# Kernel tuning notes

Measured on AMD Instinct MI355X. Metric: run time of the kernel, lower is better.

Reference implementation:

```python
import jax, jax.numpy as jnp
import numpy as np

B, CHAR_LEN, LSTM, VOCAB, NATTN = 4096, 64, 400, 73, 10

def _lstm_cell(x, h, c, W_ih, W_hh, b):
    # gates: [B, 4*LSTM] in (i, f, g, o) order, matching torch.nn.LSTMCell
    g = x @ W_ih.T + h @ W_hh.T + b
    i, f, gg, o = jnp.split(g, 4, axis=1)
    i = jax.nn.sigmoid(i); f = jax.nn.sigmoid(f)
    gg = jnp.tanh(gg); o = jax.nn.sigmoid(o)
    c_new = f * c + i * gg
    h_new = o * jnp.tanh(c_new)
    return h_new, c_new

def setup_inputs() -> dict:
    key = jax.random.key(0)
    ks = jax.random.split(key, 24)
    d = {}
    d['inputs'] = jax.random.normal(ks[0], (B, 3), jnp.float32)
    for n, k in zip(['h1','c1','h2','c2','h3','c3'], ks[1:7]):
        d[n] = jax.random.normal(k, (B, LSTM), jnp.float32) * 0.1
    d['kappa'] = jax.random.uniform(ks[7], (B, NATTN), jnp.float32) * 5.0
    d['w_prev'] = jax.random.uniform(ks[8], (B, VOCAB), jnp.float32)
    d['attention_values'] = jax.random.uniform(ks[9], (B, CHAR_LEN, VOCAB), jnp.float32)
    d['attention_lengths'] = jax.random.randint(ks[10], (B,), 1, CHAR_LEN + 1, jnp.int32)
    s = 0.05
    in1 = VOCAB + 3              # lstm1 input: [w, inputs]
    in23 = 3 + LSTM + VOCAB      # lstm2/3 input: [inputs, h, w]
    attn_in = VOCAB + 3 + LSTM
    d['W_ih1'] = jax.random.normal(ks[11], (4 * LSTM, in1), jnp.float32) * s
    d['W_hh1'] = jax.random.normal(ks[12], (4 * LSTM, LSTM), jnp.float32) * s
    d['b1'] = jax.random.normal(ks[13], (4 * LSTM,), jnp.float32) * s
    d['W_attn'] = jax.random.normal(ks[14], (3 * NATTN, attn_in), jnp.float32) * s
    d['b_attn'] = jax.random.normal(ks[15], (3 * NATTN,), jnp.float32) * s
    d['W_ih2'] = jax.random.normal(ks[16], (4 * LSTM, in23), jnp.float32) * s
    d['W_hh2'] = jax.random.normal(ks[17], (4 * LSTM, LSTM), jnp.float32) * s
    d['b2'] = jax.random.normal(ks[18], (4 * LSTM,), jnp.float32) * s
    d['W_ih3'] = jax.random.normal(ks[19], (4 * LSTM, in23), jnp.float32) * s
    d['W_hh3'] = jax.random.normal(ks[20], (4 * LSTM, LSTM), jnp.float32) * s
    d['b3'] = jax.random.normal(ks[21], (4 * LSTM,), jnp.float32) * s
    return d

def reference(inputs, h1, c1, h2, c2, h3, c3, kappa, w_prev, attention_values,
              attention_lengths, W_ih1, W_hh1, b1, W_attn, b_attn,
              W_ih2, W_hh2, b2, W_ih3, W_hh3, b3):
    char_len = attention_values.shape[1]
    # --- LSTM 1 ---
    s1_in = jnp.concatenate([w_prev, inputs], axis=1)
    h1n, c1n = _lstm_cell(s1_in, h1, c1, W_ih1, W_hh1, b1)
    # --- Gaussian-mixture location attention ---
    attn_in = jnp.concatenate([w_prev, inputs, h1n], axis=1)
    attn_params = jax.nn.softplus(attn_in @ W_attn.T + b_attn)
    alpha, beta, kap = jnp.split(attn_params, 3, axis=1)
    kap = kappa + kap / 25.0
    beta = jnp.maximum(beta, 0.01)
    u = jnp.arange(char_len, dtype=jnp.float32)[None, None, :]           # [1,1,C]
    phi = jnp.sum(alpha[:, :, None] *
                  jnp.exp(-jnp.square(kap[:, :, None] - u) / beta[:, :, None]),
                  axis=1)                                                 # [B,C]
    seq_mask = (jnp.arange(char_len)[None, :] < attention_lengths[:, None]).astype(jnp.float32)
    w = jnp.einsum('bc,bcv->bv', phi * seq_mask, attention_values)        # [B,V]
    # --- LSTM 2 & 3 ---
    s2_in = jnp.concatenate([inputs, h1n, w], axis=1)
    h2n, c2n = _lstm_cell(s2_in, h2, c2, W_ih2, W_hh2, b2)
    s3_in = jnp.concatenate([inputs, h2n, w], axis=1)
    h3n, c3n = _lstm_cell(s3_in, h3, c3, W_ih3, W_hh3, b3)
    return h3n
```

## Files before the change

kernel.cpp:

```cpp
#include <hip/hip_runtime.h>
#include <hip/hip_bf16.h>


#define B_SZ     4096
#define LSTM_N   400
#define NG       1600
#define NGP      1664
#define VOCAB    73
#define NATTN    10
#define CHARLEN  64
#define KP1      480
#define KP23     896

typedef _Float16 half8 __attribute__((ext_vector_type(8)));
typedef __attribute__((ext_vector_type(4))) float floatx4;

__device__ __forceinline__ void gload_lds16(const void* g, void* l) {
    __builtin_amdgcn_global_load_lds(
        (const __attribute__((address_space(1))) void*)g,
        (__attribute__((address_space(3))) void*)l, 16, 0, 0);
}

__device__ __forceinline__ int lds_slot(int r, int s) {
    return ((r >> 1) << 6) + (((((r & 1) << 2) | s) ^ ((r >> 1) & 7)) << 3);
}

__global__ __launch_bounds__(256) void pack_wall(const float* __restrict__ Wih1,
                                                 const float* __restrict__ Whh1,
                                                 const float* __restrict__ Wih2,
                                                 const float* __restrict__ Whh2,
                                                 const float* __restrict__ Wih3,
                                                 const float* __restrict__ Whh3,
                                                 const float* __restrict__ W_attn,
                                                 _Float16* __restrict__ W1,
                                                 _Float16* __restrict__ W2,
                                                 _Float16* __restrict__ W3,
                                                 _Float16* __restrict__ Wa)
{
    const int z = blockIdx.z;
    const int n = blockIdx.y;
    const int k = blockIdx.x * 256 + threadIdx.x;
    if (z == 0) {
        if (k >= KP1) return;
        float v = 0.f;
        if (n < NG) {
            if (k < 76)             v = Wih1[(size_t)n * 76 + k];
            else if (k < 476)       v = Whh1[(size_t)n * 400 + (k - 76)];
        }
        W1[(size_t)n * KP1 + k] = (_Float16)v;
    } else if (z == 1 || z == 2) {
        if (k >= KP23) return;
        const float* Wih = (z == 1) ? Wih2 : Wih3;
        const float* Whh = (z == 1) ? Whh2 : Whh3;
        float v = 0.f;
        if (n < NG) {
            if (k < 476)            v = Wih[(size_t)n * 476 + k];
            else if (k < 876)       v = Whh[(size_t)n * 400 + (k - 476)];
        }
        ((z == 1) ? W2 : W3)[(size_t)n * KP23 + k] = (_Float16)v;
    } else {
        if (n >= 128 || k >= KP1) return;
        float v = (n < 30 && k < 476) ? W_attn[(size_t)n * 476 + k] : 0.f;
        Wa[(size_t)n * KP1 + k] = (_Float16)v;
    }
}

__global__ __launch_bounds__(256) void pack_x(const float* __restrict__ w_prev,
                                              const float* __restrict__ inputs,
                                              const float* __restrict__ h1,
                                              const float* __restrict__ h2,
                                              const float* __restrict__ h3,
                                              _Float16* __restrict__ X1,
                                              _Float16* __restrict__ X2,
                                              _Float16* __restrict__ X3)
{
    const int b = blockIdx.y;
    const int k = blockIdx.x * 256 + threadIdx.x;
    if (k < KP1) {
        float v = 0.f;
        if (k < 73)        v = w_prev[(size_t)b * 73 + k];
        else if (k < 76)   v = inputs[(size_t)b * 3 + (k - 73)];
        else if (k < 476)  v = h1[(size_t)b * 400 + (k - 76)];
        X1[(size_t)b * KP1 + k] = (_Float16)v;
    }
    const int kk = k - KP1;
    if (kk >= 0 && kk < KP23) {
        if (kk >= 3 && kk < 476) return;
        float v2 = 0.f, v3 = 0.f;
        if (kk < 3) { v2 = inputs[(size_t)b * 3 + kk]; v3 = v2; }
        else if (kk >= 476 && kk < 876) {
            v2 = h2[(size_t)b * 400 + (kk - 476)];
            v3 = h3[(size_t)b * 400 + (kk - 476)];
        }
        X2[(size_t)b * KP23 + kk] = (_Float16)v2;
        X3[(size_t)b * KP23 + kk] = (_Float16)v3;
    }
}

__global__ __launch_bounds__(256) void gemm_f16(const _Float16* __restrict__ A,
                                                const _Float16* __restrict__ Bw,
                                                const float* __restrict__ bias,
                                                float* __restrict__ C, int Kp,
                                                int ldC, int Nvalid)
{
    __shared__ _Float16 As[128 * 32];
    __shared__ _Float16 Bs[128 * 32];

    const int t    = threadIdx.x;
    const int w    = t >> 6;
    const int lane = t & 63;
    const int quad = lane >> 4;
    const int l16  = lane & 15;
    const int m0   = blockIdx.y * 128;
    const int n0   = blockIdx.x * 128;
    const int wm   = (w >> 1) * 64;
    const int wn   = (w & 1) * 64;
    const int pr   = lane >> 3;
    const int sw8  = (lane & 7) ^ pr;
    const int rowo = (pr << 1) + (sw8 >> 2);
    const int ko   = (sw8 & 3) << 3;

    floatx4 acc[4][4] = {};

    for (int k0 = 0; k0 < Kp; k0 += 32) {
        __syncthreads();
#pragma unroll
        for (int j = 0; j < 2; j++) {
            const int cr = (j * 4 + w) * 16;
            gload_lds16(A  + (size_t)(m0 + cr + rowo) * Kp + k0 + ko, As + cr * 32);
            gload_lds16(Bw + (size_t)(n0 + cr + rowo) * Kp + k0 + ko, Bs + cr * 32);
        }
        asm volatile("s_waitcnt vmcnt(0)" ::: "memory");
        __syncthreads();

        half8 af[4], bf[4];
#pragma unroll
        for (int i = 0; i < 4; i++) {
            af[i] = *(const half8*)(As + lds_slot(wm + i * 16 + l16, quad));
            bf[i] = *(const half8*)(Bs + lds_slot(wn + i * 16 + l16, quad));
        }
#pragma unroll
        for (int mt = 0; mt < 4; mt++)
#pragma unroll
            for (int nt = 0; nt < 4; nt++)
                acc[mt][nt] = __builtin_amdgcn_mfma_f32_16x16x32_f16(
                    af[mt], bf[nt], acc[mt][nt], 0, 0, 0);
    }

#pragma unroll
    for (int nt = 0; nt < 4; nt++) {
        const int n = n0 + wn + nt * 16 + l16;
        if (n >= Nvalid) continue;
        const float bv = bias[n];
#pragma unroll
        for (int mt = 0; mt < 4; mt++) {
            const int mbase = m0 + wm + mt * 16 + quad * 4;
#pragma unroll
            for (int r = 0; r < 4; r++)
                C[(size_t)(mbase + r) * ldC + n] = acc[mt][nt][r] + bv;
        }
    }
}

__global__ __launch_bounds__(256) void gates_mid(const float* __restrict__ G,
                                                 const float* __restrict__ c_in,
                                                 _Float16* __restrict__ d1, int ld1,
                                                 _Float16* __restrict__ d2, int ld2)
{
    int id = blockIdx.x * 256 + threadIdx.x;
    if (id >= B_SZ * LSTM_N) return;
    int b = id / LSTM_N;
    int u = id - b * LSTM_N;
    const float* g = G + (size_t)b * NG;
    float gi = g[u], gf = g[LSTM_N + u], gc = g[2 * LSTM_N + u], go = g[3 * LSTM_N + u];
    float si = 1.f / (1.f + expf(-gi));
    float sf = 1.f / (1.f + expf(-gf));
    float so = 1.f / (1.f + expf(-go));
    float cn = sf * c_in[id] + si * tanhf(gc);
    float h  = so * tanhf(cn);
    _Float16 hh = (_Float16)h;
    d1[(size_t)b * ld1 + u] = hh;
    if (d2) d2[(size_t)b * ld2 + u] = hh;
}

__global__ __launch_bounds__(256) void gates_last(const float* __restrict__ G,
                                                  const float* __restrict__ c_in,
                                                  float* __restrict__ out)
{
    int id = blockIdx.x * 256 + threadIdx.x;
    if (id >= B_SZ * LSTM_N) return;
    int b = id / LSTM_N;
    int u = id - b * LSTM_N;
    const float* g = G + (size_t)b * NG;
    float gi = g[u], gf = g[LSTM_N + u], gc = g[2 * LSTM_N + u], go = g[3 * LSTM_N + u];
    float si = 1.f / (1.f + expf(-gi));
    float sf = 1.f / (1.f + expf(-gf));
    float so = 1.f / (1.f + expf(-go));
    float cn = sf * c_in[id] + si * tanhf(gc);
    out[id]  = so * tanhf(cn);
}

__global__ __launch_bounds__(256) void attn_phi(const float* __restrict__ AP,
                                                const float* __restrict__ kappa,
                                                const float* __restrict__ AV,
                                                const int* __restrict__ alen,
                                                _Float16* __restrict__ X2,
                                                _Float16* __restrict__ X3)
{
    __shared__ float prm[4][32];
    __shared__ float phi_s[4][CHARLEN];

    const int t = threadIdx.x;
    const int wave = t >> 6;
    const int lane = t & 63;
    const int b = blockIdx.x * 4 + wave;

    if (lane < 30) {
        float p  = AP[(size_t)b * 32 + lane];
        float sp = (p > 20.f) ? p : log1pf(expf(p));
        float v;
        if (lane < 10)      v = sp;
        else if (lane < 20) v = fmaxf(sp, 0.01f);
        else                v = kappa[(size_t)b * NATTN + (lane - 20)] + sp * (1.f / 25.f);
        prm[wave][lane] = v;
    }
    __syncthreads();

    const int len = alen[b];
    {
        int c = lane;
        float phi = 0.f;
#pragma unroll
        for (int j = 0; j < NATTN; j++) {
            float d = prm[wave][20 + j] - (float)c;
            phi += prm[wave][j] * expf(-d * d / prm[wave][10 + j]);
        }
        phi_s[wave][c] = (c < len) ? phi : 0.f;
    }
    __syncthreads();

    for (int v0 = 0; v0 < VOCAB; v0 += 64) {
        const int v = v0 + lane;
        if (v < VOCAB) {
            const float* avb = AV + (size_t)b * CHARLEN * VOCAB + v;
            float s = 0.f;
            for (int c = 0; c < len; c++)
                s += phi_s[wave][c] * avb[(size_t)c * VOCAB];
            _Float16 wv = (_Float16)s;
            X2[(size_t)b * KP23 + 403 + v] = wv;
            X3[(size_t)b * KP23 + 403 + v] = wv;
        }
    }
}

extern "C" void kernel_launch(void* const* d_in, const int* in_sizes, int n_in,
                              void* d_out, int out_size, void* d_ws, size_t ws_size,
                              hipStream_t stream)
{
    const float* inputs = (const float*)d_in[0];
    const float* h1     = (const float*)d_in[1];
    const float* c1     = (const float*)d_in[2];
    const float* h2     = (const float*)d_in[3];
    const float* c2     = (const float*)d_in[4];
    const float* h3     = (const float*)d_in[5];
    const float* c3     = (const float*)d_in[6];
    const float* kappa  = (const float*)d_in[7];
    const float* w_prev = (const float*)d_in[8];
    const float* AV     = (const float*)d_in[9];
    const int*   alen   = (const int*)d_in[10];
    const float* W_ih1  = (const float*)d_in[11];
    const float* W_hh1  = (const float*)d_in[12];
    const float* b1     = (const float*)d_in[13];
    const float* W_attn = (const float*)d_in[14];
    const float* b_attn = (const float*)d_in[15];
    const float* W_ih2  = (const float*)d_in[16];
    const float* W_hh2  = (const float*)d_in[17];
    const float* b2     = (const float*)d_in[18];
    const float* W_ih3  = (const float*)d_in[19];
    const float* W_hh3  = (const float*)d_in[20];
    const float* b3     = (const float*)d_in[21];
    float* out = (float*)d_out;

    char* p = (char*)d_ws;
    _Float16* X1 = (_Float16*)p; p += (size_t)B_SZ * KP1 * 2;
    _Float16* X2 = (_Float16*)p; p += (size_t)B_SZ * KP23 * 2;
    _Float16* X3 = (_Float16*)p; p += (size_t)B_SZ * KP23 * 2;
    _Float16* W1 = (_Float16*)p; p += (size_t)NGP * KP1 * 2;
    _Float16* W2 = (_Float16*)p; p += (size_t)NGP * KP23 * 2;
    _Float16* W3 = (_Float16*)p; p += (size_t)NGP * KP23 * 2;
    _Float16* Wa = (_Float16*)p; p += (size_t)128 * KP1 * 2;
    float* AP = (float*)p; p += (size_t)B_SZ * 32 * 4;
    float* G  = (float*)p;

    pack_wall<<<dim3(4, NGP, 4), 256, 0, stream>>>(W_ih1, W_hh1, W_ih2, W_hh2,
                                                   W_ih3, W_hh3, W_attn,
                                                   W1, W2, W3, Wa);
    pack_x<<<dim3((KP1 + KP23 + 255) / 256, B_SZ), 256, 0, stream>>>(
        w_prev, inputs, h1, h2, h3, X1, X2, X3);

    const int gates_blocks = (B_SZ * LSTM_N + 255) / 256;
    const dim3 gemm_grid(NGP / 128, B_SZ / 128);

    gemm_f16<<<gemm_grid, 256, 0, stream>>>(X1, W1, b1, G, KP1, NG, NG);
    gates_mid<<<gates_blocks, 256, 0, stream>>>(G, c1, X2 + 3, KP23, X1 + 76, KP1);
    gemm_f16<<<dim3(1, B_SZ / 128), 256, 0, stream>>>(X1, Wa, b_attn, AP, KP1, 32, 30);
    attn_phi<<<B_SZ / 4, 256, 0, stream>>>(AP, kappa, AV, alen, X2, X3);
    gemm_f16<<<gemm_grid, 256, 0, stream>>>(X2, W2, b2, G, KP23, NG, NG);
    gates_mid<<<gates_blocks, 256, 0, stream>>>(G, c2, X3 + 3, KP23, nullptr, 0);
    gemm_f16<<<gemm_grid, 256, 0, stream>>>(X3, W3, b3, G, KP23, NG, NG);
    gates_last<<<gates_blocks, 256, 0, stream>>>(G, c3, out);
}
```

Baseline: 337.1 us.

## Fuse LSTM gate nonlinearities into GEMM epilogue via interleaved gate-row weight layout

Weight rows are repacked so each unit's i,f,g,o gates sit in four consecutive rows, and the GEMM is transposed (weights as M, batch as N). The accumulator's four values per lane then hold all four gates of one unit, so the cell update runs in the GEMM epilogue and the gates_mid/gates_last kernels and the fp32 gate buffer G go away. A separate XA buffer is added so the attention GEMM reads the new h1 without racing the fused LSTM1 writes into X1. The epilogue stores are strided across batch rows with 16-bit and scalar writes, which may coalesce poorly.

```diff
diff --git a/kernel.cpp b/kernel.cpp
--- a/kernel.cpp
+++ b/kernel.cpp
@@ -40,28 +40,32 @@
     const int z = blockIdx.z;
     const int n = blockIdx.y;
     const int k = blockIdx.x * 256 + threadIdx.x;
+    if (z == 3) {
+        if (n >= 128 || k >= KP1) return;
+        float v = (n < 30 && k < 476) ? W_attn[(size_t)n * 476 + k] : 0.f;
+        Wa[(size_t)n * KP1 + k] = (_Float16)v;
+        return;
+    }
+    const int u = n >> 2, g = n & 3;
+    const int src = g * 400 + u;
     if (z == 0) {
         if (k >= KP1) return;
         float v = 0.f;
-        if (n < NG) {
-            if (k < 76)             v = Wih1[(size_t)n * 76 + k];
-            else if (k < 476)       v = Whh1[(size_t)n * 400 + (k - 76)];
+        if (u < 400) {
+            if (k < 76)           v = Wih1[(size_t)src * 76 + k];
+            else if (k < 476)     v = Whh1[(size_t)src * 400 + (k - 76)];
         }
         W1[(size_t)n * KP1 + k] = (_Float16)v;
-    } else if (z == 1 || z == 2) {
+    } else {
         if (k >= KP23) return;
         const float* Wih = (z == 1) ? Wih2 : Wih3;
         const float* Whh = (z == 1) ? Whh2 : Whh3;
         float v = 0.f;
-        if (n < NG) {
-            if (k < 476)            v = Wih[(size_t)n * 476 + k];
-            else if (k < 876)       v = Whh[(size_t)n * 400 + (k - 476)];
+        if (u < 400) {
+            if (k < 476)          v = Wih[(size_t)src * 476 + k];
+            else if (k < 876)     v = Whh[(size_t)src * 400 + (k - 476)];
         }
         ((z == 1) ? W2 : W3)[(size_t)n * KP23 + k] = (_Float16)v;
-    } else {
-        if (n >= 128 || k >= KP1) return;
-        float v = (n < 30 && k < 476) ? W_attn[(size_t)n * 476 + k] : 0.f;
-        Wa[(size_t)n * KP1 + k] = (_Float16)v;
     }
 }
 
@@ -71,6 +75,7 @@
                                               const float* __restrict__ h2,
                                               const float* __restrict__ h3,
                                               _Float16* __restrict__ X1,
+                                              _Float16* __restrict__ XA,
                                               _Float16* __restrict__ X2,
                                               _Float16* __restrict__ X3)
 {
@@ -82,6 +87,7 @@
         else if (k < 76)   v = inputs[(size_t)b * 3 + (k - 73)];
         else if (k < 476)  v = h1[(size_t)b * 400 + (k - 76)];
         X1[(size_t)b * KP1 + k] = (_Float16)v;
+        if (k < 76 || k >= 476) XA[(size_t)b * KP1 + k] = (_Float16)v;
     }
     const int kk = k - KP1;
     if (kk >= 0 && kk < KP23) {
@@ -97,11 +103,13 @@
     }
 }
 
-__global__ __launch_bounds__(256) void gemm_f16(const _Float16* __restrict__ A,
-                                                const _Float16* __restrict__ Bw,
-                                                const float* __restrict__ bias,
-                                                float* __restrict__ C, int Kp,
-                                                int ldC, int Nvalid)
+__global__ __launch_bounds__(256) void gemm_fused(const _Float16* __restrict__ Wm,
+                                                  const _Float16* __restrict__ X,
+                                                  const float* __restrict__ bias,
+                                                  const float* __restrict__ c_in,
+                                                  _Float16* __restrict__ d1, int ld1,
+                                                  _Float16* __restrict__ d2, int ld2,
+                                                  float* __restrict__ fout, int Kp)
 {
     __shared__ _Float16 As[128 * 32];
     __shared__ _Float16 Bs[128 * 32];
@@ -127,6 +135,87 @@
 #pragma unroll
         for (int j = 0; j < 2; j++) {
             const int cr = (j * 4 + w) * 16;
+            gload_lds16(Wm + (size_t)(m0 + cr + rowo) * Kp + k0 + ko, As + cr * 32);
+            gload_lds16(X  + (size_t)(n0 + cr + rowo) * Kp + k0 + ko, Bs + cr * 32);
+        }
+        asm volatile("s_waitcnt vmcnt(0)" ::: "memory");
+        __syncthreads();
+
+        half8 af[4], bf[4];
+#pragma unroll
+        for (int i = 0; i < 4; i++) {
+            af[i] = *(const half8*)(As + lds_slot(wm + i * 16 + l16, quad));
+            bf[i] = *(const half8*)(Bs + lds_slot(wn + i * 16 + l16, quad));
+        }
+#pragma unroll
+        for (int mt = 0; mt < 4; mt++)
+#pragma unroll
+            for (int nt = 0; nt < 4; nt++)
+                acc[mt][nt] = __builtin_amdgcn_mfma_f32_16x16x32_f16(
+                    af[mt], bf[nt], acc[mt][nt], 0, 0, 0);
+    }
+
+#pragma unroll
+    for (int mt = 0; mt < 4; mt++) {
+        const int u = ((m0 + wm + mt * 16) >> 2) + quad;
+        if (u >= LSTM_N) continue;
+        const float bi = bias[u];
+        const float bff = bias[400 + u];
+        const float bg = bias[800 + u];
+        const float bo = bias[1200 + u];
+#pragma unroll
+        for (int nt = 0; nt < 4; nt++) {
+            const int b = n0 + wn + nt * 16 + l16;
+            float gi = acc[mt][nt][0] + bi;
+            float gf = acc[mt][nt][1] + bff;
+            float gg = acc[mt][nt][2] + bg;
+            float go = acc[mt][nt][3] + bo;
+            float si = 1.f / (1.f + expf(-gi));
+            float sf = 1.f / (1.f + expf(-gf));
+            float so = 1.f / (1.f + expf(-go));
+            float cn = sf * c_in[(size_t)b * LSTM_N + u] + si * tanhf(gg);
+            float h  = so * tanhf(cn);
+            if (fout) {
+                fout[(size_t)b * LSTM_N + u] = h;
+            } else {
+                _Float16 hh = (_Float16)h;
+                d1[(size_t)b * ld1 + u] = hh;
+                if (d2) d2[(size_t)b * ld2 + u] = hh;
+            }
+        }
+    }
+}
+
+__global__ __launch_bounds__(256) void gemm_plain(const _Float16* __restrict__ A,
+                                                  const _Float16* __restrict__ Bw,
+                                                  const float* __restrict__ bias,
+                                                  float* __restrict__ C, int Kp,
+                                                  int ldC, int Nvalid)
+{
+    __shared__ _Float16 As[128 * 32];
+    __shared__ _Float16 Bs[128 * 32];
+
+    const int t    = threadIdx.x;
+    const int w    = t >> 6;
+    const int lane = t & 63;
+    const int quad = lane >> 4;
+    const int l16  = lane & 15;
+    const int m0   = blockIdx.y * 128;
+    const int n0   = blockIdx.x * 128;
+    const int wm   = (w >> 1) * 64;
+    const int wn   = (w & 1) * 64;
+    const int pr   = lane >> 3;
+    const int sw8  = (lane & 7) ^ pr;
+    const int rowo = (pr << 1) + (sw8 >> 2);
+    const int ko   = (sw8 & 3) << 3;
+
+    floatx4 acc[4][4] = {};
+
+    for (int k0 = 0; k0 < Kp; k0 += 32) {
+        __syncthreads();
+#pragma unroll
+        for (int j = 0; j < 2; j++) {
+            const int cr = (j * 4 + w) * 16;
             gload_lds16(A  + (size_t)(m0 + cr + rowo) * Kp + k0 + ko, As + cr * 32);
             gload_lds16(Bw + (size_t)(n0 + cr + rowo) * Kp + k0 + ko, Bs + cr * 32);
         }
@@ -160,44 +249,6 @@
                 C[(size_t)(mbase + r) * ldC + n] = acc[mt][nt][r] + bv;
         }
     }
-}
-
-__global__ __launch_bounds__(256) void gates_mid(const float* __restrict__ G,
-                                                 const float* __restrict__ c_in,
-                                                 _Float16* __restrict__ d1, int ld1,
-                                                 _Float16* __restrict__ d2, int ld2)
-{
-    int id = blockIdx.x * 256 + threadIdx.x;
-    if (id >= B_SZ * LSTM_N) return;
-    int b = id / LSTM_N;
-    int u = id - b * LSTM_N;
-    const float* g = G + (size_t)b * NG;
-    float gi = g[u], gf = g[LSTM_N + u], gc = g[2 * LSTM_N + u], go = g[3 * LSTM_N + u];
-    float si = 1.f / (1.f + expf(-gi));
-    float sf = 1.f / (1.f + expf(-gf));
-    float so = 1.f / (1.f + expf(-go));
-    float cn = sf * c_in[id] + si * tanhf(gc);
-    float h  = so * tanhf(cn);
-    _Float16 hh = (_Float16)h;
-    d1[(size_t)b * ld1 + u] = hh;
-    if (d2) d2[(size_t)b * ld2 + u] = hh;
-}
-
-__global__ __launch_bounds__(256) void gates_last(const float* __restrict__ G,
-                                                  const float* __restrict__ c_in,
-                                                  float* __restrict__ out)
-{
-    int id = blockIdx.x * 256 + threadIdx.x;
-    if (id >= B_SZ * LSTM_N) return;
-    int b = id / LSTM_N;
-    int u = id - b * LSTM_N;
-    const float* g = G + (size_t)b * NG;
-    float gi = g[u], gf = g[LSTM_N + u], gc = g[2 * LSTM_N + u], go = g[3 * LSTM_N + u];
-    float si = 1.f / (1.f + expf(-gi));
-    float sf = 1.f / (1.f + expf(-gf));
-    float so = 1.f / (1.f + expf(-go));
-    float cn = sf * c_in[id] + si * tanhf(gc);
-    out[id]  = so * tanhf(cn);
 }
 
 __global__ __launch_bounds__(256) void attn_phi(const float* __restrict__ AP,
@@ -283,30 +334,29 @@
 
     char* p = (char*)d_ws;
     _Float16* X1 = (_Float16*)p; p += (size_t)B_SZ * KP1 * 2;
+    _Float16* XA = (_Float16*)p; p += (size_t)B_SZ * KP1 * 2;
     _Float16* X2 = (_Float16*)p; p += (size_t)B_SZ * KP23 * 2;
     _Float16* X3 = (_Float16*)p; p += (size_t)B_SZ * KP23 * 2;
     _Float16* W1 = (_Float16*)p; p += (size_t)NGP * KP1 * 2;
     _Float16* W2 = (_Float16*)p; p += (size_t)NGP * KP23 * 2;
     _Float16* W3 = (_Float16*)p; p += (size_t)NGP * KP23 * 2;
     _Float16* Wa = (_Float16*)p; p += (size_t)128 * KP1 * 2;
-    float* AP = (float*)p; p += (size_t)B_SZ * 32 * 4;
-    float* G  = (float*)p;
+    float* AP = (float*)p;
 
     pack_wall<<<dim3(4, NGP, 4), 256, 0, stream>>>(W_ih1, W_hh1, W_ih2, W_hh2,
                                                    W_ih3, W_hh3, W_attn,
                                                    W1, W2, W3, Wa);
     pack_x<<<dim3((KP1 + KP23 + 255) / 256, B_SZ), 256, 0, stream>>>(
-        w_prev, inputs, h1, h2, h3, X1, X2, X3);
-
-    const int gates_blocks = (B_SZ * LSTM_N + 255) / 256;
-    const dim3 gemm_grid(NGP / 128, B_SZ / 128);
-
-    gemm_f16<<<gemm_grid, 256, 0, stream>>>(X1, W1, b1, G, KP1, NG, NG);
-    gates_mid<<<gates_blocks, 256, 0, stream>>>(G, c1, X2 + 3, KP23, X1 + 76, KP1);
-    gemm_f16<<<dim3(1, B_SZ / 128), 256, 0, stream>>>(X1, Wa, b_attn, AP, KP1, 32, 30);
+        w_prev, inputs, h1, h2, h3, X1, XA, X2, X3);
+
+    const dim3 fgrid(B_SZ / 128, NGP / 128);
+
+    gemm_fused<<<fgrid, 256, 0, stream>>>(W1, X1, b1, c1,
+                                          XA + 76, KP1, X2 + 3, KP23, nullptr, KP1);
+    gemm_plain<<<dim3(1, B_SZ / 128), 256, 0, stream>>>(XA, Wa, b_attn, AP, KP1, 32, 30);
     attn_phi<<<B_SZ / 4, 256, 0, stream>>>(AP, kappa, AV, alen, X2, X3);
-    gemm_f16<<<gemm_grid, 256, 0, stream>>>(X2, W2, b2, G, KP23, NG, NG);
-    gates_mid<<<gates_blocks, 256, 0, stream>>>(G, c2, X3 + 3, KP23, nullptr, 0);
-    gemm_f16<<<gemm_grid, 256, 0, stream>>>(X3, W3, b3, G, KP23, NG, NG);
-    gates_last<<<gates_blocks, 256, 0, stream>>>(G, c3, out);
-}
+    gemm_fused<<<fgrid, 256, 0, stream>>>(W2, X2, b2, c2,
+                                          X3 + 3, KP23, nullptr, 0, nullptr, KP23);
+    gemm_fused<<<fgrid, 256, 0, stream>>>(W3, X3, b3, c3,
+                                          nullptr, 0, nullptr, 0, out, KP23);
+}
```

Result: faster. 323.1 us (-4.1%).
